# Optimization experiments

Hardware: AMD Instinct MI355X
Metric: run time of the kernel (lower is better)

## Reference

```python
import jax, jax.numpy as jnp
import numpy as np

BATCH = 32768
TEXT_DIM = 384
HIDDEN = 256
NUM_LAYERS = 4
NUM_VERTS = 12
K_NN = 6


def _build_template():
    """Icosphere vertices (12, normalized) and row-normalized kNN adjacency (12,12)."""
    phi = (1.0 + 5.0 ** 0.5) / 2.0
    v = np.array([
        [-1, phi, 0], [1, phi, 0], [-1, -phi, 0], [1, -phi, 0],
        [0, -1, phi], [0, 1, phi], [0, -1, -phi], [0, 1, -phi],
        [phi, 0, -1], [phi, 0, 1], [-phi, 0, -1], [-phi, 0, 1],
    ], dtype=np.float32)
    v = v / np.linalg.norm(v, axis=1, keepdims=True)
    dist = np.linalg.norm(v[:, None, :] - v[None, :, :], axis=-1)  # (12,12)
    # k+1 smallest per row; index 0 is self (distance 0), skip it
    idx = np.argsort(dist, axis=1, kind='stable')[:, 1:K_NN + 1]
    adj = np.zeros((NUM_VERTS, NUM_VERTS), dtype=np.float32)
    rows = np.repeat(np.arange(NUM_VERTS), K_NN)
    adj[rows, idx.reshape(-1)] = 1.0
    adj = adj / (adj.sum(axis=1, keepdims=True) + 1e-6)
    return jnp.asarray(v), jnp.asarray(adj)


def setup_inputs() -> dict:
    key = jax.random.key(0)
    ks = jax.random.split(key, 8)
    template, adjacency = _build_template()
    scale = 0.02
    return {
        "text_emb": jax.random.normal(ks[0], (BATCH, TEXT_DIM), dtype=jnp.float32),
        "W_text": jax.random.normal(ks[1], (TEXT_DIM, HIDDEN), dtype=jnp.float32) * scale,
        "b_text": jnp.zeros((HIDDEN,), dtype=jnp.float32),
        "W_gnn": jax.random.normal(ks[2], (NUM_LAYERS, HIDDEN, HIDDEN), dtype=jnp.float32) * scale,
        "b_gnn": jnp.zeros((NUM_LAYERS, HIDDEN), dtype=jnp.float32),
        "W_out": jax.random.normal(ks[3], (HIDDEN, 3), dtype=jnp.float32) * scale,
        "b_out": jnp.zeros((3,), dtype=jnp.float32),
        "adjacency": adjacency,   # (12,12) buffer
        "template": template,     # (12,3) buffer
    }


def reference(text_emb, W_text, b_text, W_gnn, b_gnn, W_out, b_out, adjacency, template):
    # text projection -> broadcast to all nodes
    tf = text_emb @ W_text + b_text                       # (B, H)
    B = text_emb.shape[0]
    h = jnp.broadcast_to(tf[:, None, :], (B, NUM_VERTS, HIDDEN))
    # GNN layers: aggregate (shared adjacency across batch), project, relu
    for l in range(NUM_LAYERS):
        agg = jnp.einsum('nm,bmd->bnd', adjacency, h)     # (B, 12, H)
        h = jax.nn.relu(agg @ W_gnn[l] + b_gnn[l])
    displacements = h @ W_out + b_out                     # (B, 12, 3)
    return template[None, :, :] + displacements
```

## Files before the change

### kernel.cpp

```cpp
#include <hip/hip_runtime.h>
#include <stdint.h>

#define TD      384
#define HID     256

typedef __bf16 bf16;
typedef __attribute__((ext_vector_type(8))) __bf16 bf16x8;
typedef __attribute__((ext_vector_type(4))) float f32x4;

union FragU { uint4 u; bf16x8 f; };
union PackU { uint4 u; bf16 v[8]; };

__device__ inline f32x4 mfma16(bf16x8 a, bf16x8 b, f32x4 c) {
  return __builtin_amdgcn_mfma_f32_16x16x32_bf16(a, b, c, 0, 0, 0);
}

__global__ __launch_bounds__(256) void prep_wf(
    const float* __restrict__ W_text, const float* __restrict__ b_text,
    const float* __restrict__ W_gnn, const float* __restrict__ b_gnn,
    float* __restrict__ wf, float* __restrict__ bfv)
{
  int n = threadIdx.x;
  const float* g0 = W_gnn;
  if (blockIdx.x < 48) {
    int k0 = blockIdx.x * 8;
    float a[8] = {0.f,0.f,0.f,0.f,0.f,0.f,0.f,0.f};
    for (int j = 0; j < HID; j++) {
      float g = g0[(size_t)j * HID + n];
      #pragma unroll
      for (int r = 0; r < 8; r++)
        a[r] += W_text[(size_t)(k0 + r) * HID + j] * g;
    }
    #pragma unroll
    for (int r = 0; r < 8; r++) wf[(size_t)(k0 + r) * HID + n] = a[r];
  } else {
    float s = 0.f;
    for (int j = 0; j < HID; j++) s += b_text[j] * g0[(size_t)j * HID + n];
    bfv[n] = s + b_gnn[n];
  }
}

__global__ __launch_bounds__(256) void prep_pack(
    const float* __restrict__ wf, const float* __restrict__ W_gnn,
    const float* __restrict__ W_out,
    bf16* __restrict__ wt_f, bf16* __restrict__ wt_g, float* __restrict__ wot)
{
  int bid = blockIdx.x, tid = threadIdx.x;
  if (bid < 48) {
    int idx = bid * 256 + tid;
    int cc = idx & 15, c = idx >> 4;
    int n16 = c / 48, oct = c - n16 * 48;
    int n = n16 * 16 + cc;
    PackU pk;
    #pragma unroll
    for (int j = 0; j < 8; j++) pk.v[j] = (bf16)wf[(oct * 8 + j) * HID + n];
    *(uint4*)(wt_f + idx * 8) = pk.u;
  } else if (bid < 144) {
    int idx = (bid - 48) * 256 + tid;
    int cc = idx & 15, c = idx >> 4;
    int l = c >> 9, c2 = c & 511;
    int oct = c2 & 31;
    int n = (c2 >> 5) * 16 + cc;
    const float* base = W_gnn + (size_t)(l + 1) * HID * HID;
    PackU pk;
    #pragma unroll
    for (int j = 0; j < 8; j++) pk.v[j] = (bf16)base[(oct * 8 + j) * HID + n];
    *(uint4*)(wt_g + idx * 8) = pk.u;
  } else {
    for (int t = tid; t < 3 * HID; t += 256) {
      int comp = t >> 8, k = t & 255;
      wot[comp * HID + k] = W_out[k * 3 + comp];
    }
  }
}

__global__ __launch_bounds__(256, 2) void mesh_kernel(
    const float* __restrict__ text,
    const bf16* __restrict__ wt_f,
    const bf16* __restrict__ wt_g,
    const float* __restrict__ b_f,
    const float* __restrict__ b_gnn,
    const float* __restrict__ wot,
    const float* __restrict__ b_out,
    const float* __restrict__ tmpl,
    float* __restrict__ out)
{
  __shared__ __align__(16) unsigned char smem[81920];
  unsigned char* Tbuf = smem;
  unsigned char* Hbuf = smem + 49152;
  float* dispBuf = (float*)(smem + 32768);

  const int tid  = threadIdx.x;
  const int lane = tid & 63;
  const int w    = tid >> 6;
  const int cc   = lane & 15;
  const int qq   = lane >> 4;
  const int rowbase = blockIdx.x * 64;

  f32x4 acc[4][4];

  auto zero_acc = [&]() {
    f32x4 z = {0.f, 0.f, 0.f, 0.f};
    #pragma unroll
    for (int mt = 0; mt < 4; mt++)
      #pragma unroll
      for (int nt = 0; nt < 4; nt++) acc[mt][nt] = z;
  };

  auto loadA = [&](const unsigned char* src, int rowB, int ks, bf16x8* A) {
    #pragma unroll
    for (int mt = 0; mt < 4; mt++) {
      int m = mt * 16 + cc;
      FragU fu;
      fu.u = *(const uint4*)(src + m * rowB + (((ks * 4 + qq) ^ (m & 7)) * 16));
      A[mt] = fu.f;
    }
  };

  auto loadB = [&](const char* wb, int K8, int ks, bf16x8* B) {
    #pragma unroll
    for (int nt = 0; nt < 4; nt++) {
      FragU fu;
      fu.u = *(const uint4*)(wb + (size_t)(nt * K8 + ks * 4) * 256);
      B[nt] = fu.f;
    }
  };

  auto epilogue = [&](unsigned char* dst, const float* bias_ptr, bool relu) {
    float bias4[4];
    #pragma unroll
    for (int nt = 0; nt < 4; nt++) bias4[nt] = bias_ptr[w * 64 + nt * 16 + cc];
    #pragma unroll
    for (int mt = 0; mt < 4; mt++) {
      #pragma unroll
      for (int nt = 0; nt < 4; nt++) {
        int col = w * 64 + nt * 16 + cc;
        #pragma unroll
        for (int r = 0; r < 4; r++) {
          int m = mt * 16 + qq * 4 + r;
          float v = acc[mt][nt][r] + bias4[nt];
          if (relu) v = fmaxf(v, 0.f);
          *(bf16*)(dst + m * 512 + ((col >> 3) ^ (m & 7)) * 16 + (col & 7) * 2) = (bf16)v;
        }
      }
    }
  };

  auto runLayer = [&](const unsigned char* src, const char* wb,
                      unsigned char* dst, const float* bias_ptr) {
    zero_acc();
    bf16x8 A[4], B[4], An[4], Bn[4];
    loadB(wb, 32, 0, B);
    loadA(src, 512, 0, A);
    #pragma unroll
    for (int ks = 0; ks < 8; ks++) {
      if (ks < 7) {
        loadB(wb, 32, ks + 1, Bn);
        loadA(src, 512, ks + 1, An);
      }
      #pragma unroll
      for (int mt = 0; mt < 4; mt++)
        #pragma unroll
        for (int nt = 0; nt < 4; nt++)
          acc[mt][nt] = mfma16(A[mt], B[nt], acc[mt][nt]);
      if (ks < 7) {
        #pragma unroll
        for (int t = 0; t < 4; t++) { A[t] = An[t]; B[t] = Bn[t]; }
      }
    }
    epilogue(dst, bias_ptr, true);
  };

  const float* tbase = text + (size_t)rowbase * TD;
  auto stageHalf = [&](int half) {
    #pragma unroll
    for (int i = 0; i < 6; i++) {
      int id = i * 256 + tid;
      int m = id / 24, ol = id - m * 24;
      int o = half * 24 + ol;
      const float4* p = (const float4*)(tbase + m * TD + o * 8);
      float4 x = p[0], y = p[1];
      PackU pk;
      pk.v[0]=(bf16)x.x; pk.v[1]=(bf16)x.y; pk.v[2]=(bf16)x.z; pk.v[3]=(bf16)x.w;
      pk.v[4]=(bf16)y.x; pk.v[5]=(bf16)y.y; pk.v[6]=(bf16)y.z; pk.v[7]=(bf16)y.w;
      *(uint4*)(Tbuf + m * 768 + ((o ^ (m & 7)) * 16)) = pk.u;
    }
  };

  stageHalf(0);
  __syncthreads();
  stageHalf(1);

  zero_acc();
  const char* wbf = (const char*)wt_f + (size_t)(w * 4 * 48 + qq) * 256 + cc * 16;
  {
    bf16x8 A[4], B[4], An[4], Bn[4];
    loadB(wbf, 48, 0, B);
    loadA(Tbuf, 768, 0, A);
    #pragma unroll
    for (int ks = 0; ks < 6; ks++) {
      if (ks < 5) { loadB(wbf, 48, ks + 1, Bn); loadA(Tbuf, 768, ks + 1, An); }
      #pragma unroll
      for (int mt = 0; mt < 4; mt++)
        #pragma unroll
        for (int nt = 0; nt < 4; nt++)
          acc[mt][nt] = mfma16(A[mt], B[nt], acc[mt][nt]);
      if (ks < 5) {
        #pragma unroll
        for (int t = 0; t < 4; t++) { A[t] = An[t]; B[t] = Bn[t]; }
      }
    }
    __syncthreads();
    loadB(wbf, 48, 6, B);
    loadA(Tbuf, 768, 6, A);
    #pragma unroll
    for (int ks = 6; ks < 12; ks++) {
      if (ks < 11) { loadB(wbf, 48, ks + 1, Bn); loadA(Tbuf, 768, ks + 1, An); }
      #pragma unroll
      for (int mt = 0; mt < 4; mt++)
        #pragma unroll
        for (int nt = 0; nt < 4; nt++)
          acc[mt][nt] = mfma16(A[mt], B[nt], acc[mt][nt]);
      if (ks < 11) {
        #pragma unroll
        for (int t = 0; t < 4; t++) { A[t] = An[t]; B[t] = Bn[t]; }
      }
    }
  }
  epilogue(Hbuf, b_f, true);
  __syncthreads();

  {
    const char* wg = (const char*)wt_g + (size_t)(w * 4 * 32 + qq) * 256 + cc * 16;
    runLayer(Hbuf, wg,                          Tbuf, b_gnn + 1 * HID);
    __syncthreads();
    runLayer(Tbuf, wg + (size_t)1 * HID * HID * 2, Hbuf, b_gnn + 2 * HID);
    __syncthreads();
    runLayer(Hbuf, wg + (size_t)2 * HID * HID * 2, Tbuf, b_gnn + 3 * HID);
    __syncthreads();
  }

  if (tid < 192) {
    int comp = tid >> 6;
    int r = tid & 63;
    const float4* wrow = (const float4*)(wot + comp * HID);
    float s = 0.f;
    #pragma unroll 4
    for (int o = 0; o < 32; o++) {
      FragU fu; fu.u = *(const uint4*)(Tbuf + r * 512 + ((o ^ (r & 7)) * 16));
      float4 w0 = wrow[2 * o], w1 = wrow[2 * o + 1];
      s += (float)fu.f[0]*w0.x + (float)fu.f[1]*w0.y + (float)fu.f[2]*w0.z + (float)fu.f[3]*w0.w;
      s += (float)fu.f[4]*w1.x + (float)fu.f[5]*w1.y + (float)fu.f[6]*w1.z + (float)fu.f[7]*w1.w;
    }
    dispBuf[r * 3 + comp] = s + b_out[comp];
  }
  __syncthreads();

  #pragma unroll
  for (int ii = 0; ii < 9; ii++) {
    int i = ii * 256 + tid;
    int row = i / 36;
    int j = i - row * 36;
    out[(size_t)rowbase * 36 + i] = tmpl[j] + dispBuf[row * 3 + j % 3];
  }
}

extern "C" void kernel_launch(void* const* d_in, const int* in_sizes, int n_in,
                              void* d_out, int out_size, void* d_ws, size_t ws_size,
                              hipStream_t stream) {
  const float* text   = (const float*)d_in[0];
  const float* W_text = (const float*)d_in[1];
  const float* b_text = (const float*)d_in[2];
  const float* W_gnn  = (const float*)d_in[3];
  const float* b_gnn  = (const float*)d_in[4];
  const float* W_out  = (const float*)d_in[5];
  const float* b_out  = (const float*)d_in[6];
  const float* tmpl   = (const float*)d_in[8];
  float* outp = (float*)d_out;

  float* wf   = (float*)d_ws;
  float* bfv  = wf + TD * HID;
  float* wot  = bfv + HID;
  bf16* wt_f  = (bf16*)(wot + 3 * HID);
  bf16* wt_g  = wt_f + TD * HID;

  prep_wf<<<49, 256, 0, stream>>>(W_text, b_text, W_gnn, b_gnn, wf, bfv);
  prep_pack<<<145, 256, 0, stream>>>(wf, W_gnn, W_out, wt_f, wt_g, wot);
  mesh_kernel<<<32768 / 64, 256, 0, stream>>>(text, wt_f, wt_g, bfv, b_gnn,
                                              wot, b_out, tmpl, outp);
}
```

Measured before the change: 144.2 us.

## Merge weight prep kernels and deepen B-fragment prefetch in MFMA loops

Fuses the two weight-preparation kernels into one launch that computes the folded W_text·W_gnn[0] product and packs it directly to bf16 layout, dropping the fp32 intermediate buffer and one launch. In the main kernel, the B (weight) fragments are now prefetched two k-steps ahead instead of one to hide global load latency. The output projection uses four partial accumulators to break the serial dependency chain. The deeper prefetch costs extra registers, which may pressure occupancy at the two-blocks-per-CU launch bound.

```diff
diff --git a/kernel.cpp b/kernel.cpp
--- a/kernel.cpp
+++ b/kernel.cpp
@@ -15,45 +15,37 @@
   return __builtin_amdgcn_mfma_f32_16x16x32_bf16(a, b, c, 0, 0, 0);
 }
 
-__global__ __launch_bounds__(256) void prep_wf(
+__global__ __launch_bounds__(256) void prep_all(
     const float* __restrict__ W_text, const float* __restrict__ b_text,
     const float* __restrict__ W_gnn, const float* __restrict__ b_gnn,
-    float* __restrict__ wf, float* __restrict__ bfv)
+    const float* __restrict__ W_out,
+    bf16* __restrict__ wt_f, bf16* __restrict__ wt_g,
+    float* __restrict__ wot, float* __restrict__ bfv)
 {
-  int n = threadIdx.x;
+  const int bid = blockIdx.x, tid = threadIdx.x;
   const float* g0 = W_gnn;
-  if (blockIdx.x < 48) {
-    int k0 = blockIdx.x * 8;
-    float a[8] = {0.f,0.f,0.f,0.f,0.f,0.f,0.f,0.f};
-    for (int j = 0; j < HID; j++) {
-      float g = g0[(size_t)j * HID + n];
-      #pragma unroll
-      for (int r = 0; r < 8; r++)
-        a[r] += W_text[(size_t)(k0 + r) * HID + j] * g;
-    }
-    #pragma unroll
-    for (int r = 0; r < 8; r++) wf[(size_t)(k0 + r) * HID + n] = a[r];
-  } else {
-    float s = 0.f;
-    for (int j = 0; j < HID; j++) s += b_text[j] * g0[(size_t)j * HID + n];
-    bfv[n] = s + b_gnn[n];
-  }
-}
-
-__global__ __launch_bounds__(256) void prep_pack(
-    const float* __restrict__ wf, const float* __restrict__ W_gnn,
-    const float* __restrict__ W_out,
-    bf16* __restrict__ wt_f, bf16* __restrict__ wt_g, float* __restrict__ wot)
-{
-  int bid = blockIdx.x, tid = threadIdx.x;
   if (bid < 48) {
-    int idx = bid * 256 + tid;
-    int cc = idx & 15, c = idx >> 4;
-    int n16 = c / 48, oct = c - n16 * 48;
-    int n = n16 * 16 + cc;
+    const int k0 = bid * 8;
+    const int n = tid;
+    float a0=0.f,a1=0.f,a2=0.f,a3=0.f,a4=0.f,a5=0.f,a6=0.f,a7=0.f;
+    for (int j = 0; j < HID; j += 8) {
+      #pragma unroll
+      for (int u = 0; u < 8; u++) {
+        float g = g0[(size_t)(j + u) * HID + n];
+        a0 += W_text[(size_t)(k0 + 0) * HID + j + u] * g;
+        a1 += W_text[(size_t)(k0 + 1) * HID + j + u] * g;
+        a2 += W_text[(size_t)(k0 + 2) * HID + j + u] * g;
+        a3 += W_text[(size_t)(k0 + 3) * HID + j + u] * g;
+        a4 += W_text[(size_t)(k0 + 4) * HID + j + u] * g;
+        a5 += W_text[(size_t)(k0 + 5) * HID + j + u] * g;
+        a6 += W_text[(size_t)(k0 + 6) * HID + j + u] * g;
+        a7 += W_text[(size_t)(k0 + 7) * HID + j + u] * g;
+      }
+    }
     PackU pk;
-    #pragma unroll
-    for (int j = 0; j < 8; j++) pk.v[j] = (bf16)wf[(oct * 8 + j) * HID + n];
+    pk.v[0]=(bf16)a0; pk.v[1]=(bf16)a1; pk.v[2]=(bf16)a2; pk.v[3]=(bf16)a3;
+    pk.v[4]=(bf16)a4; pk.v[5]=(bf16)a5; pk.v[6]=(bf16)a6; pk.v[7]=(bf16)a7;
+    int idx = ((n >> 4) * 48 + bid) * 16 + (n & 15);
     *(uint4*)(wt_f + idx * 8) = pk.u;
   } else if (bid < 144) {
     int idx = (bid - 48) * 256 + tid;
@@ -67,6 +59,14 @@
     for (int j = 0; j < 8; j++) pk.v[j] = (bf16)base[(oct * 8 + j) * HID + n];
     *(uint4*)(wt_g + idx * 8) = pk.u;
   } else {
+    int n = tid;
+    float s0 = 0.f, s1 = 0.f;
+    for (int j = 0; j < HID; j += 2) {
+      s0 += b_text[j]     * g0[(size_t)j * HID + n];
+      s1 += b_text[j + 1] * g0[(size_t)(j + 1) * HID + n];
+    }
+    bfv[n] = s0 + s1 + b_gnn[n];
+    #pragma unroll
     for (int t = tid; t < 3 * HID; t += 256) {
       int comp = t >> 8, k = t & 255;
       wot[comp * HID + k] = W_out[k * 3 + comp];
@@ -149,23 +149,28 @@
   auto runLayer = [&](const unsigned char* src, const char* wb,
                       unsigned char* dst, const float* bias_ptr) {
     zero_acc();
-    bf16x8 A[4], B[4], An[4], Bn[4];
-    loadB(wb, 32, 0, B);
+    bf16x8 A[4], An[4], B0[4], B1[4], B2[4];
+    loadB(wb, 32, 0, B0);
+    loadB(wb, 32, 1, B1);
     loadA(src, 512, 0, A);
     #pragma unroll
     for (int ks = 0; ks < 8; ks++) {
+      if (ks < 6) loadB(wb, 32, ks + 2, B2);
+      if (ks < 7) loadA(src, 512, ks + 1, An);
+      #pragma unroll
+      for (int mt = 0; mt < 4; mt++)
+        #pragma unroll
+        for (int nt = 0; nt < 4; nt++)
+          acc[mt][nt] = mfma16(A[mt], B0[nt], acc[mt][nt]);
+      #pragma unroll
+      for (int t = 0; t < 4; t++) B0[t] = B1[t];
+      if (ks < 6) {
+        #pragma unroll
+        for (int t = 0; t < 4; t++) B1[t] = B2[t];
+      }
       if (ks < 7) {
-        loadB(wb, 32, ks + 1, Bn);
-        loadA(src, 512, ks + 1, An);
-      }
-      #pragma unroll
-      for (int mt = 0; mt < 4; mt++)
-        #pragma unroll
-        for (int nt = 0; nt < 4; nt++)
-          acc[mt][nt] = mfma16(A[mt], B[nt], acc[mt][nt]);
-      if (ks < 7) {
-        #pragma unroll
-        for (int t = 0; t < 4; t++) { A[t] = An[t]; B[t] = Bn[t]; }
+        #pragma unroll
+        for (int t = 0; t < 4; t++) A[t] = An[t];
       }
     }
     epilogue(dst, bias_ptr, true);
@@ -194,36 +199,46 @@
   zero_acc();
   const char* wbf = (const char*)wt_f + (size_t)(w * 4 * 48 + qq) * 256 + cc * 16;
   {
-    bf16x8 A[4], B[4], An[4], Bn[4];
-    loadB(wbf, 48, 0, B);
+    bf16x8 A[4], An[4], B0[4], B1[4], B2[4];
+    loadB(wbf, 48, 0, B0);
+    loadB(wbf, 48, 1, B1);
     loadA(Tbuf, 768, 0, A);
     #pragma unroll
     for (int ks = 0; ks < 6; ks++) {
-      if (ks < 5) { loadB(wbf, 48, ks + 1, Bn); loadA(Tbuf, 768, ks + 1, An); }
+      loadB(wbf, 48, ks + 2, B2);
+      if (ks < 5) loadA(Tbuf, 768, ks + 1, An);
       #pragma unroll
       for (int mt = 0; mt < 4; mt++)
         #pragma unroll
         for (int nt = 0; nt < 4; nt++)
-          acc[mt][nt] = mfma16(A[mt], B[nt], acc[mt][nt]);
+          acc[mt][nt] = mfma16(A[mt], B0[nt], acc[mt][nt]);
+      #pragma unroll
+      for (int t = 0; t < 4; t++) { B0[t] = B1[t]; B1[t] = B2[t]; }
       if (ks < 5) {
         #pragma unroll
-        for (int t = 0; t < 4; t++) { A[t] = An[t]; B[t] = Bn[t]; }
+        for (int t = 0; t < 4; t++) A[t] = An[t];
       }
     }
     __syncthreads();
-    loadB(wbf, 48, 6, B);
     loadA(Tbuf, 768, 6, A);
     #pragma unroll
     for (int ks = 6; ks < 12; ks++) {
-      if (ks < 11) { loadB(wbf, 48, ks + 1, Bn); loadA(Tbuf, 768, ks + 1, An); }
+      if (ks < 10) loadB(wbf, 48, ks + 2, B2);
+      if (ks < 11) loadA(Tbuf, 768, ks + 1, An);
       #pragma unroll
       for (int mt = 0; mt < 4; mt++)
         #pragma unroll
         for (int nt = 0; nt < 4; nt++)
-          acc[mt][nt] = mfma16(A[mt], B[nt], acc[mt][nt]);
+          acc[mt][nt] = mfma16(A[mt], B0[nt], acc[mt][nt]);
+      #pragma unroll
+      for (int t = 0; t < 4; t++) B0[t] = B1[t];
+      if (ks < 10) {
+        #pragma unroll
+        for (int t = 0; t < 4; t++) B1[t] = B2[t];
+      }
       if (ks < 11) {
         #pragma unroll
-        for (int t = 0; t < 4; t++) { A[t] = An[t]; B[t] = Bn[t]; }
+        for (int t = 0; t < 4; t++) A[t] = An[t];
       }
     }
   }
@@ -244,15 +259,18 @@
     int comp = tid >> 6;
     int r = tid & 63;
     const float4* wrow = (const float4*)(wot + comp * HID);
-    float s = 0.f;
-    #pragma unroll 4
+    float sacc[4] = {0.f, 0.f, 0.f, 0.f};
+    #pragma unroll
     for (int o = 0; o < 32; o++) {
       FragU fu; fu.u = *(const uint4*)(Tbuf + r * 512 + ((o ^ (r & 7)) * 16));
       float4 w0 = wrow[2 * o], w1 = wrow[2 * o + 1];
-      s += (float)fu.f[0]*w0.x + (float)fu.f[1]*w0.y + (float)fu.f[2]*w0.z + (float)fu.f[3]*w0.w;
-      s += (float)fu.f[4]*w1.x + (float)fu.f[5]*w1.y + (float)fu.f[6]*w1.z + (float)fu.f[7]*w1.w;
-    }
-    dispBuf[r * 3 + comp] = s + b_out[comp];
+      float t0 = (float)fu.f[0]*w0.x + (float)fu.f[1]*w0.y
+               + (float)fu.f[2]*w0.z + (float)fu.f[3]*w0.w
+               + (float)fu.f[4]*w1.x + (float)fu.f[5]*w1.y
+               + (float)fu.f[6]*w1.z + (float)fu.f[7]*w1.w;
+      sacc[o & 3] += t0;
+    }
+    dispBuf[r * 3 + comp] = (sacc[0] + sacc[1]) + (sacc[2] + sacc[3]) + b_out[comp];
   }
   __syncthreads();
 
@@ -278,14 +296,13 @@
   const float* tmpl   = (const float*)d_in[8];
   float* outp = (float*)d_out;
 
-  float* wf   = (float*)d_ws;
-  float* bfv  = wf + TD * HID;
+  float* bfv  = (float*)d_ws;
   float* wot  = bfv + HID;
   bf16* wt_f  = (bf16*)(wot + 3 * HID);
   bf16* wt_g  = wt_f + TD * HID;
 
-  prep_wf<<<49, 256, 0, stream>>>(W_text, b_text, W_gnn, b_gnn, wf, bfv);
-  prep_pack<<<145, 256, 0, stream>>>(wf, W_gnn, W_out, wt_f, wt_g, wot);
+  prep_all<<<145, 256, 0, stream>>>(W_text, b_text, W_gnn, b_gnn, W_out,
+                                    wt_f, wt_g, wot, bfv);
   mesh_kernel<<<32768 / 64, 256, 0, stream>>>(text, wt_f, wt_g, bfv, b_gnn,
                                               wot, b_out, tmpl, outp);
 }
```

Result: faster. 139.2 us (-3.5%).
